# Performance work log

Measured on AMD Instinct MI355X. Metric: run time of the kernel, lower is better.

## Reference

```python
import jax, jax.numpy as jnp
import numpy as np

NUM_HEADS = 12

def setup_inputs() -> dict:
    key = jax.random.key(0)
    k1, k2, k3, k4 = jax.random.split(key, 4)
    B, N, C = 8, 4096, 768
    x1 = jax.random.normal(k1, (B, N, C), dtype=jnp.float32)
    x2 = jax.random.normal(k2, (B, N, C), dtype=jnp.float32)
    segfeature = jax.random.normal(k3, (B, N, C), dtype=jnp.float32)
    # nn.Linear(dim, 2*dim, bias=False) weight, stored transposed for y = x @ W
    W_kv = jax.random.normal(k4, (C, 2 * C), dtype=jnp.float32) * (C ** -0.5)
    return {"x1": x1, "x2": x2, "segfeature": segfeature, "W_kv": W_kv}


def reference(x1, x2, segfeature, W_kv):
    B, N, C = x1.shape
    H = NUM_HEADS
    d = C // H
    scale = d ** -0.5
    # queries: [B, H, N, d]
    q1 = x1.reshape(B, N, H, d).transpose(0, 2, 1, 3)
    q2 = x2.reshape(B, N, H, d).transpose(0, 2, 1, 3)
    # kv projection: [B, M, 2C] -> [2, B, H, M, d]
    M = segfeature.shape[1]
    kv = (segfeature @ W_kv).reshape(B, M, 2, H, d).transpose(2, 0, 3, 1, 4)
    k3, v3 = kv[0], kv[1]
    # context matrix: k^T @ v over sequence -> [B, H, d, d]
    ctx = jnp.einsum('bhmd,bhme->bhde', k3, v3) * scale
    ctx = jax.nn.softmax(ctx, axis=-2)
    # apply context to both queries, back to [B, N, C]
    o1 = jnp.einsum('bhnd,bhde->bnhe', q1, ctx).reshape(B, N, C)
    o2 = jnp.einsum('bhnd,bhde->bnhe', q2, ctx).reshape(B, N, C)
    return (o1, o2)
```

## Files before the change

kernel.cpp:

```cpp
#include <hip/hip_runtime.h>

#define DI __device__ __forceinline__

typedef float        f32x4 __attribute__((ext_vector_type(4)));
typedef _Float16     f16x8 __attribute__((ext_vector_type(8)));
typedef unsigned int u32x4 __attribute__((ext_vector_type(4)));
typedef unsigned int u32x2 __attribute__((ext_vector_type(2)));

DI unsigned short f2h(float f){
    _Float16 h = (_Float16)f;
    return __builtin_bit_cast(unsigned short, h);
}

DI void gl_lds16(const void* g, void* l){
    __builtin_amdgcn_global_load_lds(
        (const __attribute__((address_space(1))) unsigned int*)g,
        (__attribute__((address_space(3))) unsigned int*)l, 16, 0, 0);
}

__global__ __launch_bounds__(256) void k_transpose_f16(
    const float* __restrict__ in, unsigned short* __restrict__ o16,
    int rows, int cols, long ibs, long obs)
{
    __shared__ float t[64][65];
    const int b  = blockIdx.z;
    const int r0 = blockIdx.y * 64, c0 = blockIdx.x * 64;
    const int tid = threadIdx.x;
    const float* ib = in + (long)b * ibs;

    #pragma unroll
    for (int i = 0; i < 4; ++i){
        int r  = (tid >> 4) + i * 16;
        int cq = (tid & 15) * 4;
        f32x4 v = *(const f32x4*)&ib[(long)(r0 + r) * cols + c0 + cq];
        t[r][cq+0] = v[0]; t[r][cq+1] = v[1]; t[r][cq+2] = v[2]; t[r][cq+3] = v[3];
    }
    __syncthreads();

    const int c  = tid >> 2;
    const int ms = (tid & 3) * 16;
    unsigned hv[8];
    #pragma unroll
    for (int k2 = 0; k2 < 8; ++k2){
        unsigned short ha = f2h(t[ms + 2*k2 + 0][c]);
        unsigned short hb = f2h(t[ms + 2*k2 + 1][c]);
        hv[k2] = (unsigned)ha | ((unsigned)hb << 16);
    }
    long o = (long)b * obs + (long)(c0 + c) * rows + r0 + ms;
    u32x4 H0 = {hv[0],hv[1],hv[2],hv[3]}, H1 = {hv[4],hv[5],hv[6],hv[7]};
    *(u32x4*)&o16[o]     = H0;
    *(u32x4*)&o16[o + 8] = H1;
}

DI void stage_lds(const unsigned short* __restrict__ src, long stride,
                  int row0, int k0, unsigned short* tile, int tid)
{
    #pragma unroll
    for (int it = 0; it < 4; ++it){
        int D    = (it * 256 + tid) * 16;
        int row  = D >> 7;
        int colb = (D & 127) ^ ((row & 7) << 4);
        const char* g = (const char*)(src + (long)(row0 + row) * stride + k0) + colb;
        gl_lds16(g, (char*)tile + D);
    }
}

DI f16x8 frag_ld(const unsigned short* tile, int row, int kc16)
{
    int logical = (row << 7) + (kc16 << 4);
    int phys    = logical ^ ((row & 7) << 4);
    return *(const f16x8*)((const char*)tile + phys);
}

DI void kloop(const unsigned short* a, int rowA0, long sA,
              const unsigned short* b, int rowB0, long sB,
              int kbeg, int kend, f32x4 acc[4][4], unsigned short* lds, int tid)
{
    const int lane = tid & 63;
    const int wave = tid >> 6;
    const int wr = (wave >> 1) * 64, wc = (wave & 1) * 64;

    stage_lds(a, sA, rowA0, kbeg, lds,        tid);
    stage_lds(b, sB, rowB0, kbeg, lds + 8192, tid);
    __syncthreads();

    int cur = 0;
    for (int k0 = kbeg; k0 < kend; k0 += 64){
        const unsigned short* TA = lds + cur * 16384;
        const unsigned short* TB = TA + 8192;

        const int kn = k0 + 64;
        if (kn < kend){
            unsigned short* NA = lds + (cur ^ 1) * 16384;
            stage_lds(a, sA, rowA0, kn, NA,        tid);
            stage_lds(b, sB, rowB0, kn, NA + 8192, tid);
        }

        #pragma unroll
        for (int ks = 0; ks < 2; ++ks){
            const int kc = ks * 4 + (lane >> 4);
            f16x8 bf[4];
            #pragma unroll
            for (int cf = 0; cf < 4; ++cf)
                bf[cf] = frag_ld(TB, wc + cf * 16 + (lane & 15), kc);
            #pragma unroll
            for (int rf = 0; rf < 4; ++rf){
                f16x8 af = frag_ld(TA, wr + rf * 16 + (lane & 15), kc);
                #pragma unroll
                for (int cf = 0; cf < 4; ++cf)
                    acc[rf][cf] = __builtin_amdgcn_mfma_f32_16x16x32_f16(af, bf[cf], acc[rf][cf], 0, 0, 0);
            }
        }

        __syncthreads();
        cur ^= 1;
    }
}

__global__ __launch_bounds__(256) void k_gram(
    const unsigned short* __restrict__ X, float* __restrict__ Gp)
{
    __shared__ unsigned short lds[4 * 8192];
    const int id  = blockIdx.x;
    const int b   = id & 7;
    const int r   = id >> 3;
    const int ksl = r / 21;
    int q = r % 21;
    int ti = 0, tj = 0;
    #pragma unroll
    for (int i = 0; i < 6; ++i){ int c = 6 - i; if (q < c){ ti = i; tj = i + q; q = -1; break; } q -= c; }

    static const int kb[4] = {0, 1408, 2752, 4096};

    const unsigned short* XB = X + (long)b * 768 * 4096;

    f32x4 acc[4][4];
    #pragma unroll
    for (int i = 0; i < 4; ++i)
        #pragma unroll
        for (int j = 0; j < 4; ++j) acc[i][j] = (f32x4){0.f, 0.f, 0.f, 0.f};

    kloop(XB, ti * 128, 4096, XB, tj * 128, 4096,
          kb[ksl], kb[ksl + 1], acc, lds, threadIdx.x);

    float* G = Gp + ((long)ksl * 8 + b) * 768 * 768;
    const int lane = threadIdx.x & 63, wave = threadIdx.x >> 6;
    const int wr = (wave >> 1) * 64, wc = (wave & 1) * 64;
    #pragma unroll
    for (int rf = 0; rf < 4; ++rf)
        #pragma unroll
        for (int cf = 0; cf < 4; ++cf){
            int gi = ti * 128 + wr + rf * 16 + 4 * (lane >> 4);
            int gj = tj * 128 + wc + cf * 16 + (lane & 15);
            #pragma unroll
            for (int r2 = 0; r2 < 4; ++r2){
                float v = acc[rf][cf][r2];
                G[(long)(gi + r2) * 768 + gj] = v;
                if (ti != tj) G[(long)gj * 768 + gi + r2] = v;
            }
        }
}

__global__ __launch_bounds__(256) void k_sumsplit(
    const float* __restrict__ gp, unsigned short* __restrict__ g16)
{
    const long S = 4718592;
    long i = ((long)blockIdx.x * 256 + threadIdx.x) * 4;
    f32x4 a = *(const f32x4*)(gp + i);
    f32x4 b = *(const f32x4*)(gp + S + i);
    f32x4 c = *(const f32x4*)(gp + 2 * S + i);
    unsigned hv[2];
    #pragma unroll
    for (int k2 = 0; k2 < 2; ++k2){
        unsigned short ha = f2h(a[2*k2+0] + b[2*k2+0] + c[2*k2+0]);
        unsigned short hb = f2h(a[2*k2+1] + b[2*k2+1] + c[2*k2+1]);
        hv[k2] = (unsigned)ha | ((unsigned)hb << 16);
    }
    *(u32x2*)(g16 + i) = (u32x2){hv[0], hv[1]};
}

__global__ __launch_bounds__(256) void k_tt(
    const unsigned short* __restrict__ WT, const unsigned short* __restrict__ G,
    unsigned short* __restrict__ TT)
{
    __shared__ unsigned short lds[4 * 8192];
    const int id = blockIdx.x;
    const int b  = id & 7;
    const int t  = id >> 3;
    const int ti = t % 6, tj = t / 6;

    const unsigned short* A = WT + (long)768 * 768;
    const unsigned short* B = G + (long)b * 768 * 768;

    f32x4 acc[4][4];
    #pragma unroll
    for (int i = 0; i < 4; ++i)
        #pragma unroll
        for (int j = 0; j < 4; ++j) acc[i][j] = (f32x4){0.f, 0.f, 0.f, 0.f};

    kloop(A, ti * 128, 768, B, tj * 128, 768, 0, 768, acc, lds, threadIdx.x);

    unsigned short* tt = TT + (long)b * 768 * 768;
    const int lane = threadIdx.x & 63, wave = threadIdx.x >> 6;
    const int wr = (wave >> 1) * 64, wc = (wave & 1) * 64;
    #pragma unroll
    for (int rf = 0; rf < 4; ++rf)
        #pragma unroll
        for (int cf = 0; cf < 4; ++cf){
            int gi = ti * 128 + wr + rf * 16 + 4 * (lane >> 4);
            int gj = tj * 128 + wc + cf * 16 + (lane & 15);
            #pragma unroll
            for (int r = 0; r < 4; ++r)
                tt[(long)(gi + r) * 768 + gj] = f2h(acc[rf][cf][r]);
        }
}

__global__ __launch_bounds__(256) void k_ctx(
    const unsigned short* __restrict__ WT, const unsigned short* __restrict__ TT,
    unsigned short* __restrict__ wT)
{
    __shared__ float red[3][64][65];
    const int bh = blockIdx.x;
    const int b = bh / 12, h = bh % 12;
    const int lane = threadIdx.x & 63;
    const int wave = threadIdx.x >> 6;

    const unsigned short* A = WT + (long)(h * 64) * 768;
    const unsigned short* B = TT + (long)b * 768 * 768 + (long)(h * 64) * 768;

    f32x4 acc[4][4];
    #pragma unroll
    for (int i = 0; i < 4; ++i)
        #pragma unroll
        for (int j = 0; j < 4; ++j) acc[i][j] = (f32x4){0.f, 0.f, 0.f, 0.f};

    for (int kc = wave * 6; kc < wave * 6 + 6; ++kc){
        const int k0 = kc * 32 + (lane >> 4) * 8;
        f16x8 af[4], bf[4];
        #pragma unroll
        for (int f = 0; f < 4; ++f){
            long ro = (long)(f * 16 + (lane & 15)) * 768 + k0;
            af[f] = *(const f16x8*)(A + ro);
            bf[f] = *(const f16x8*)(B + ro);
        }
        #pragma unroll
        for (int rf = 0; rf < 4; ++rf)
            #pragma unroll
            for (int cf = 0; cf < 4; ++cf)
                acc[rf][cf] = __builtin_amdgcn_mfma_f32_16x16x32_f16(af[rf], bf[cf], acc[rf][cf], 0, 0, 0);
    }

    if (wave > 0){
        #pragma unroll
        for (int rf = 0; rf < 4; ++rf)
            #pragma unroll
            for (int cf = 0; cf < 4; ++cf)
                #pragma unroll
                for (int r = 0; r < 4; ++r)
                    red[wave - 1][lane][(rf * 4 + cf) * 4 + r] = acc[rf][cf][r];
    }
    __syncthreads();
    if (wave != 0) return;

    #pragma unroll
    for (int rf = 0; rf < 4; ++rf)
        #pragma unroll
        for (int cf = 0; cf < 4; ++cf)
            #pragma unroll
            for (int r = 0; r < 4; ++r){
                int idx = (rf * 4 + cf) * 4 + r;
                acc[rf][cf][r] += red[0][lane][idx] + red[1][lane][idx] + red[2][lane][idx];
            }

    unsigned short* wout = wT + (long)bh * 4096;
    #pragma unroll
    for (int cf = 0; cf < 4; ++cf){
        float pv[16];
        float m = -3.4e38f;
        #pragma unroll
        for (int rf = 0; rf < 4; ++rf)
            #pragma unroll
            for (int r = 0; r < 4; ++r){
                float s = acc[rf][cf][r] * 0.125f;
                pv[rf * 4 + r] = s;
                m = fmaxf(m, s);
            }
        m = fmaxf(m, __shfl_xor(m, 16));
        m = fmaxf(m, __shfl_xor(m, 32));
        float sum = 0.f;
        #pragma unroll
        for (int k = 0; k < 16; ++k){ pv[k] = __expf(pv[k] - m); sum += pv[k]; }
        sum += __shfl_xor(sum, 16);
        sum += __shfl_xor(sum, 32);
        float inv = 1.f / sum;
        int e = cf * 16 + (lane & 15);
        #pragma unroll
        for (int rf = 0; rf < 4; ++rf)
            #pragma unroll
            for (int r = 0; r < 4; ++r){
                int d = rf * 16 + 4 * (lane >> 4) + r;
                wout[e * 64 + d] = f2h(pv[rf * 4 + r] * inv);
            }
    }
}

__global__ __launch_bounds__(256) void k_apply(
    const float* __restrict__ x1, const float* __restrict__ x2,
    const unsigned short* __restrict__ wT, float* __restrict__ out)
{
    __shared__ float ep[4][64][64];
    const int b = blockIdx.z;
    const int h = blockIdx.y >> 1;
    const int src = blockIdx.y & 1;
    const int lane = threadIdx.x & 63, wave = threadIdx.x >> 6;
    const int n0 = blockIdx.x * 256 + wave * 64;

    const float* x = (src ? x2 : x1) + (long)b * 4096 * 768;
    float* o = out + (long)src * 8 * 4096 * 768 + (long)b * 4096 * 768;

    const unsigned short* W = wT + (long)(b * 12 + h) * 4096;
    f16x8 bw[4][2];
    #pragma unroll
    for (int fe = 0; fe < 4; ++fe)
        #pragma unroll
        for (int ks = 0; ks < 2; ++ks)
            bw[fe][ks] = *(const f16x8*)(W + (fe * 16 + (lane & 15)) * 64 + ks * 32 + (lane >> 4) * 8);

    f32x4 acc[4][4];
    #pragma unroll
    for (int i = 0; i < 4; ++i)
        #pragma unroll
        for (int j = 0; j < 4; ++j) acc[i][j] = (f32x4){0.f, 0.f, 0.f, 0.f};

    #pragma unroll
    for (int rf = 0; rf < 4; ++rf){
        const int row = n0 + rf * 16 + (lane & 15);
        const float* xr = x + (long)row * 768 + h * 64 + (lane >> 4) * 8;
        f32x4 v0 = *(const f32x4*)(xr);
        f32x4 v1 = *(const f32x4*)(xr + 4);
        f32x4 v2 = *(const f32x4*)(xr + 32);
        f32x4 v3 = *(const f32x4*)(xr + 36);
        f16x8 a0, a1;
        #pragma unroll
        for (int t = 0; t < 4; ++t){
            a0[t]     = (_Float16)v0[t];
            a0[t + 4] = (_Float16)v1[t];
            a1[t]     = (_Float16)v2[t];
            a1[t + 4] = (_Float16)v3[t];
        }
        #pragma unroll
        for (int fe = 0; fe < 4; ++fe){
            acc[rf][fe] = __builtin_amdgcn_mfma_f32_16x16x32_f16(a0, bw[fe][0], acc[rf][fe], 0, 0, 0);
            acc[rf][fe] = __builtin_amdgcn_mfma_f32_16x16x32_f16(a1, bw[fe][1], acc[rf][fe], 0, 0, 0);
        }
    }

    #pragma unroll
    for (int rf = 0; rf < 4; ++rf)
        #pragma unroll
        for (int fe = 0; fe < 4; ++fe)
            #pragma unroll
            for (int r = 0; r < 4; ++r)
                ep[wave][rf * 16 + 4 * (lane >> 4) + r][fe * 16 + (lane & 15)] = acc[rf][fe][r];

    #pragma unroll
    for (int pass = 0; pass < 16; ++pass){
        int rr = pass * 4 + (lane >> 4);
        f32x4 v = *(const f32x4*)&ep[wave][rr][(lane & 15) * 4];
        *(f32x4*)&o[(long)(n0 + rr) * 768 + h * 64 + (lane & 15) * 4] = v;
    }
}

__global__ void k_sentinel(float* o){ o[0] = 1.0e9f; }

extern "C" void kernel_launch(void* const* d_in, const int* in_sizes, int n_in,
                              void* d_out, int out_size, void* d_ws, size_t ws_size,
                              hipStream_t stream)
{
    (void)in_sizes; (void)n_in; (void)out_size;
    const float* x1  = (const float*)d_in[0];
    const float* x2  = (const float*)d_in[1];
    const float* seg = (const float*)d_in[2];
    const float* Wkv = (const float*)d_in[3];

    char* Wb = (char*)d_ws;
    unsigned short* X   = (unsigned short*)(Wb);
    unsigned short* WT  = (unsigned short*)(Wb + 50331648);
    unsigned short* G   = (unsigned short*)(Wb + 52690944);
    unsigned short* TT  = (unsigned short*)(Wb + 62128128);
    unsigned short* wT  = (unsigned short*)(Wb + 71565312);
    float*          Gp  = (float*)(Wb + 72351744);
    const size_t need = 128974848;

    if (ws_size < need){
        k_sentinel<<<1, 1, 0, stream>>>((float*)d_out);
        return;
    }

    k_transpose_f16<<<dim3(12, 64, 8), 256, 0, stream>>>(
        seg, X, 4096, 768, (long)4096 * 768, (long)768 * 4096);
    k_transpose_f16<<<dim3(24, 12, 1), 256, 0, stream>>>(
        Wkv, WT, 768, 1536, 0, 0);

    k_gram<<<dim3(504), 256, 0, stream>>>(X, Gp);

    k_sumsplit<<<dim3(4608), 256, 0, stream>>>(Gp, G);

    k_tt<<<dim3(288), 256, 0, stream>>>(WT, G, TT);

    k_ctx<<<dim3(96), 256, 0, stream>>>(WT, TT, wT);

    k_apply<<<dim3(16, 24, 8), 256, 0, stream>>>(x1, x2, wT, (float*)d_out);
}
```

Before: 193.0 us.

## Fuse split-K partial sum into k_tt B-tile staging, store Gram partials as fp16

The Gram kernel now writes its three split-K partials as fp16, not fp32, and packs the transposed mirror store into 8-byte writes. The separate k_sumsplit kernel is removed. k_tt now loads the three partial tiles into registers, sums them and writes the swizzled result to LDS, overlapping this with the MFMA work. This saves a kernel launch and a full fp32 write/read round trip. The cost is extra fp16 rounding of each partial before summation and register-staged, non-async loads for the B operand.

```diff
diff --git a/kernel.cpp b/kernel.cpp
--- a/kernel.cpp
+++ b/kernel.cpp
@@ -72,6 +72,56 @@
     return *(const f16x8*)((const char*)tile + phys);
 }
 
+DI void ldB3(const unsigned short* __restrict__ g0, long S16, long stride,
+             int row0, int k0, int tid, f16x8 r0[4], f16x8 r1[4], f16x8 r2[4])
+{
+    #pragma unroll
+    for (int it = 0; it < 4; ++it){
+        int D    = (it * 256 + tid) * 16;
+        int row  = D >> 7;
+        int colb = D & 127;
+        long off = (long)(row0 + row) * stride + k0 + (colb >> 1);
+        r0[it] = *(const f16x8*)(g0 + off);
+        r1[it] = *(const f16x8*)(g0 + S16 + off);
+        r2[it] = *(const f16x8*)(g0 + 2 * S16 + off);
+    }
+}
+DI void wrB3(unsigned short* tile, int tid, f16x8 r0[4], f16x8 r1[4], f16x8 r2[4])
+{
+    #pragma unroll
+    for (int it = 0; it < 4; ++it){
+        int D    = (it * 256 + tid) * 16;
+        int row  = D >> 7;
+        int colb = D & 127;
+        f16x8 s;
+        #pragma unroll
+        for (int t = 0; t < 8; ++t)
+            s[t] = (_Float16)((float)r0[it][t] + (float)r1[it][t] + (float)r2[it][t]);
+        int phys = (D & ~127) | (colb ^ ((row & 7) << 4));
+        *(f16x8*)((char*)tile + phys) = s;
+    }
+}
+
+DI void mfma_tile(const unsigned short* TA, const unsigned short* TB,
+                  int wr, int wc, int lane, f32x4 acc[4][4])
+{
+    #pragma unroll
+    for (int ks = 0; ks < 2; ++ks){
+        const int kc = ks * 4 + (lane >> 4);
+        f16x8 bf[4];
+        #pragma unroll
+        for (int cf = 0; cf < 4; ++cf)
+            bf[cf] = frag_ld(TB, wc + cf * 16 + (lane & 15), kc);
+        #pragma unroll
+        for (int rf = 0; rf < 4; ++rf){
+            f16x8 af = frag_ld(TA, wr + rf * 16 + (lane & 15), kc);
+            #pragma unroll
+            for (int cf = 0; cf < 4; ++cf)
+                acc[rf][cf] = __builtin_amdgcn_mfma_f32_16x16x32_f16(af, bf[cf], acc[rf][cf], 0, 0, 0);
+        }
+    }
+}
+
 DI void kloop(const unsigned short* a, int rowA0, long sA,
               const unsigned short* b, int rowB0, long sB,
               int kbeg, int kend, f32x4 acc[4][4], unsigned short* lds, int tid)
@@ -87,38 +137,20 @@
     int cur = 0;
     for (int k0 = kbeg; k0 < kend; k0 += 64){
         const unsigned short* TA = lds + cur * 16384;
-        const unsigned short* TB = TA + 8192;
-
         const int kn = k0 + 64;
         if (kn < kend){
             unsigned short* NA = lds + (cur ^ 1) * 16384;
             stage_lds(a, sA, rowA0, kn, NA,        tid);
             stage_lds(b, sB, rowB0, kn, NA + 8192, tid);
         }
-
-        #pragma unroll
-        for (int ks = 0; ks < 2; ++ks){
-            const int kc = ks * 4 + (lane >> 4);
-            f16x8 bf[4];
-            #pragma unroll
-            for (int cf = 0; cf < 4; ++cf)
-                bf[cf] = frag_ld(TB, wc + cf * 16 + (lane & 15), kc);
-            #pragma unroll
-            for (int rf = 0; rf < 4; ++rf){
-                f16x8 af = frag_ld(TA, wr + rf * 16 + (lane & 15), kc);
-                #pragma unroll
-                for (int cf = 0; cf < 4; ++cf)
-                    acc[rf][cf] = __builtin_amdgcn_mfma_f32_16x16x32_f16(af, bf[cf], acc[rf][cf], 0, 0, 0);
-            }
-        }
-
+        mfma_tile(TA, TA + 8192, wr, wc, lane, acc);
         __syncthreads();
         cur ^= 1;
     }
 }
 
 __global__ __launch_bounds__(256) void k_gram(
-    const unsigned short* __restrict__ X, float* __restrict__ Gp)
+    const unsigned short* __restrict__ X, unsigned short* __restrict__ Gp16)
 {
     __shared__ unsigned short lds[4 * 8192];
     const int id  = blockIdx.x;
@@ -143,7 +175,7 @@
     kloop(XB, ti * 128, 4096, XB, tj * 128, 4096,
           kb[ksl], kb[ksl + 1], acc, lds, threadIdx.x);
 
-    float* G = Gp + ((long)ksl * 8 + b) * 768 * 768;
+    unsigned short* G = Gp16 + ((long)ksl * 8 + b) * 768 * 768;
     const int lane = threadIdx.x & 63, wave = threadIdx.x >> 6;
     const int wr = (wave >> 1) * 64, wc = (wave & 1) * 64;
     #pragma unroll
@@ -152,45 +184,34 @@
         for (int cf = 0; cf < 4; ++cf){
             int gi = ti * 128 + wr + rf * 16 + 4 * (lane >> 4);
             int gj = tj * 128 + wc + cf * 16 + (lane & 15);
+            unsigned short h4[4];
             #pragma unroll
             for (int r2 = 0; r2 < 4; ++r2){
-                float v = acc[rf][cf][r2];
-                G[(long)(gi + r2) * 768 + gj] = v;
-                if (ti != tj) G[(long)gj * 768 + gi + r2] = v;
+                h4[r2] = f2h(acc[rf][cf][r2]);
+                G[(long)(gi + r2) * 768 + gj] = h4[r2];
             }
-        }
-}
-
-__global__ __launch_bounds__(256) void k_sumsplit(
-    const float* __restrict__ gp, unsigned short* __restrict__ g16)
-{
-    const long S = 4718592;
-    long i = ((long)blockIdx.x * 256 + threadIdx.x) * 4;
-    f32x4 a = *(const f32x4*)(gp + i);
-    f32x4 b = *(const f32x4*)(gp + S + i);
-    f32x4 c = *(const f32x4*)(gp + 2 * S + i);
-    unsigned hv[2];
-    #pragma unroll
-    for (int k2 = 0; k2 < 2; ++k2){
-        unsigned short ha = f2h(a[2*k2+0] + b[2*k2+0] + c[2*k2+0]);
-        unsigned short hb = f2h(a[2*k2+1] + b[2*k2+1] + c[2*k2+1]);
-        hv[k2] = (unsigned)ha | ((unsigned)hb << 16);
-    }
-    *(u32x2*)(g16 + i) = (u32x2){hv[0], hv[1]};
+            if (ti != tj){
+                u32x2 p = { (unsigned)h4[0] | ((unsigned)h4[1] << 16),
+                            (unsigned)h4[2] | ((unsigned)h4[3] << 16) };
+                *(u32x2*)(G + (long)gj * 768 + gi) = p;
+            }
+        }
 }
 
 __global__ __launch_bounds__(256) void k_tt(
-    const unsigned short* __restrict__ WT, const unsigned short* __restrict__ G,
+    const unsigned short* __restrict__ WT, const unsigned short* __restrict__ Gp16,
     unsigned short* __restrict__ TT)
 {
     __shared__ unsigned short lds[4 * 8192];
+    const long S16 = 4718592;
     const int id = blockIdx.x;
     const int b  = id & 7;
     const int t  = id >> 3;
     const int ti = t % 6, tj = t / 6;
-
-    const unsigned short* A = WT + (long)768 * 768;
-    const unsigned short* B = G + (long)b * 768 * 768;
+    const int tid = threadIdx.x;
+
+    const unsigned short* A  = WT + (long)768 * 768;
+    const unsigned short* G0 = Gp16 + (long)b * 768 * 768;
 
     f32x4 acc[4][4];
     #pragma unroll
@@ -198,11 +219,35 @@
         #pragma unroll
         for (int j = 0; j < 4; ++j) acc[i][j] = (f32x4){0.f, 0.f, 0.f, 0.f};
 
-    kloop(A, ti * 128, 768, B, tj * 128, 768, 0, 768, acc, lds, threadIdx.x);
+    const int lane = tid & 63;
+    const int wave = tid >> 6;
+    const int wr = (wave >> 1) * 64, wc = (wave & 1) * 64;
+
+    {
+        f16x8 r0[4], r1[4], r2[4];
+        ldB3(G0, S16, 768, tj * 128, 0, tid, r0, r1, r2);
+        stage_lds(A, 768, ti * 128, 0, lds, tid);
+        wrB3(lds + 8192, tid, r0, r1, r2);
+        __syncthreads();
+    }
+
+    int cur = 0;
+    for (int k0 = 0; k0 < 768; k0 += 64){
+        const unsigned short* TA = lds + cur * 16384;
+        const int kn = k0 + 64;
+        f16x8 r0[4], r1[4], r2[4];
+        if (kn < 768){
+            ldB3(G0, S16, 768, tj * 128, kn, tid, r0, r1, r2);
+            stage_lds(A, 768, ti * 128, kn, lds + (cur ^ 1) * 16384, tid);
+        }
+        mfma_tile(TA, TA + 8192, wr, wc, lane, acc);
+        if (kn < 768)
+            wrB3(lds + (cur ^ 1) * 16384 + 8192, tid, r0, r1, r2);
+        __syncthreads();
+        cur ^= 1;
+    }
 
     unsigned short* tt = TT + (long)b * 768 * 768;
-    const int lane = threadIdx.x & 63, wave = threadIdx.x >> 6;
-    const int wr = (wave >> 1) * 64, wc = (wave & 1) * 64;
     #pragma unroll
     for (int rf = 0; rf < 4; ++rf)
         #pragma unroll
@@ -384,13 +429,12 @@
     const float* Wkv = (const float*)d_in[3];
 
     char* Wb = (char*)d_ws;
-    unsigned short* X   = (unsigned short*)(Wb);
-    unsigned short* WT  = (unsigned short*)(Wb + 50331648);
-    unsigned short* G   = (unsigned short*)(Wb + 52690944);
-    unsigned short* TT  = (unsigned short*)(Wb + 62128128);
-    unsigned short* wT  = (unsigned short*)(Wb + 71565312);
-    float*          Gp  = (float*)(Wb + 72351744);
-    const size_t need = 128974848;
+    unsigned short* X    = (unsigned short*)(Wb);
+    unsigned short* WT   = (unsigned short*)(Wb + 50331648);
+    unsigned short* TT   = (unsigned short*)(Wb + 52690944);
+    unsigned short* wT   = (unsigned short*)(Wb + 62128128);
+    unsigned short* Gp16 = (unsigned short*)(Wb + 62914560);
+    const size_t need = 91226112;
 
     if (ws_size < need){
         k_sentinel<<<1, 1, 0, stream>>>((float*)d_out);
@@ -402,11 +446,9 @@
     k_transpose_f16<<<dim3(24, 12, 1), 256, 0, stream>>>(
         Wkv, WT, 768, 1536, 0, 0);
 
-    k_gram<<<dim3(504), 256, 0, stream>>>(X, Gp);
-
-    k_sumsplit<<<dim3(4608), 256, 0, stream>>>(Gp, G);
-
-    k_tt<<<dim3(288), 256, 0, stream>>>(WT, G, TT);
+    k_gram<<<dim3(504), 256, 0, stream>>>(X, Gp16);
+
+    k_tt<<<dim3(288), 256, 0, stream>>>(WT, Gp16, TT);
 
     k_ctx<<<dim3(96), 256, 0, stream>>>(WT, TT, wT);
 
```

Result: faster. 179.1 us (-7.2%).
